# Performance work log

Measured on AMD Instinct MI355X. Metric: run time of the kernel, lower is better.

## Reference

```python
import jax, jax.numpy as jnp
import numpy as np

N_NODES = 100_000
N_EDGES = 3_200_000
IN_DIM, HID_DIM, EMB_DIM = 128, 64, 32


def setup_inputs() -> dict:
    key = jax.random.key(0)
    k0, k1, k2, k3, k4, k5 = jax.random.split(key, 6)
    x = jax.random.normal(k0, (N_NODES, IN_DIM), dtype=jnp.float32)
    edge_index = jax.random.randint(k1, (2, N_EDGES), 0, N_NODES, dtype=jnp.int32)
    # GCNConv parameters (glorot-ish scale)
    W1 = jax.random.normal(k2, (IN_DIM, HID_DIM), dtype=jnp.float32) / np.sqrt(IN_DIM)
    b1 = jnp.zeros((HID_DIM,), dtype=jnp.float32)
    W2 = jax.random.normal(k3, (HID_DIM, EMB_DIM), dtype=jnp.float32) / np.sqrt(HID_DIM)
    b2 = jnp.zeros((EMB_DIM,), dtype=jnp.float32)
    return {"x": x, "W1": W1, "b1": b1, "W2": W2, "b2": b2, "edge_index": edge_index}


def reference(x, W1, b1, W2, b2, edge_index):
    """Two-layer GCN encoder (PyG GCNConv semantics, eval mode so dropout is a no-op).

    Each GCNConv: add self-loops, symmetric deg^-1/2 normalization,
    out = scatter_add(norm_e * (x @ W)[src], dst) + b.
    """
    N = x.shape[0]
    loops = jnp.arange(N, dtype=edge_index.dtype)
    src = jnp.concatenate([edge_index[0], loops])  # [E+N]
    dst = jnp.concatenate([edge_index[1], loops])  # [E+N]

    # degree of destination nodes (self-loops guarantee deg >= 1)
    deg = jax.ops.segment_sum(jnp.ones_like(dst, dtype=jnp.float32), dst,
                              num_segments=N)
    dinv = jax.lax.rsqrt(deg)                      # deg^-1/2, finite since deg>=1
    norm = dinv[src] * dinv[dst]                   # [E+N]

    def gcn_conv(h, W, b):
        h = h @ W                                  # dense transform [N, D_out]
        msg = h[src] * norm[:, None]               # gather + scale [E+N, D_out]
        return jax.ops.segment_sum(msg, dst, num_segments=N) + b

    h = jax.nn.relu(gcn_conv(x, W1, b1))
    # F.dropout with training=False is identity -> omitted
    return gcn_conv(h, W2, b2)
```

## Files before the change

### kernel.cpp

```cpp
#include <hip/hip_runtime.h>

static constexpr int NN = 100000;
static constexpr int NE = 3200000;
static constexpr int DI = 128;
static constexpr int DH = 64;
static constexpr int DO = 32;

static constexpr int NBK  = 391;
static constexpr int BCAP = 9216;
static constexpr int TILE = 8192;
static constexpr int XW1_BASE = 392;
static constexpr int XW1_BLOCKS = (NN + 63) / 64;

typedef short short8 __attribute__((ext_vector_type(8)));
typedef float f32x4  __attribute__((ext_vector_type(4)));

__device__ __forceinline__ unsigned short f2bf(float f) {
    union { float f; unsigned u; } v; v.f = f;
    unsigned r = v.u + 0x7FFFu + ((v.u >> 16) & 1u);
    return (unsigned short)(r >> 16);
}
__device__ __forceinline__ float bflo(unsigned u) {
    union { unsigned u; float f; } v; v.u = u << 16; return v.f;
}
__device__ __forceinline__ float bfhi(unsigned u) {
    union { unsigned u; float f; } v; v.u = u & 0xFFFF0000u; return v.f;
}

__global__ void k_zero(int* __restrict__ p, int n) {
    int i = blockIdx.x * blockDim.x + threadIdx.x;
    if (i < n) p[i] = 0;
}

__global__ __launch_bounds__(256) void k_mega(
        const int* __restrict__ src, const int* __restrict__ dst,
        int* __restrict__ bcur, int* __restrict__ bstore,
        const float* __restrict__ x, const float* __restrict__ W1,
        const float* __restrict__ W2,
        unsigned short* __restrict__ w2bf, unsigned short* __restrict__ h1b) {
    __shared__ int hist[NBK];
    __shared__ int lcur[NBK];
    __shared__ int gpos[NBK];
    __shared__ int stage[TILE];
    __shared__ unsigned short bid[TILE];

    int tid = threadIdx.x;

    if (blockIdx.x < NBK) {
        for (int i = tid; i < NBK; i += 256) hist[i] = 0;
        __syncthreads();

        int base = blockIdx.x * TILE;
        int p[32]; unsigned short bb[32];
#pragma unroll
        for (int k = 0; k < 32; ++k) {
            int e = base + k * 256 + tid;
            if (e < NE) {
                int d = dst[e], s = src[e];
                bb[k] = (unsigned short)(d >> 8);
                p[k]  = ((d & 255) << 24) | s;
                atomicAdd(&hist[bb[k]], 1);
            } else bb[k] = 0xFFFF;
        }
        __syncthreads();

        for (int i = tid; i < NBK; i += 256)
            gpos[i] = atomicAdd(&bcur[i], hist[i]);
        __syncthreads();

        if (tid < 64) {
            int carry = 0;
            for (int c = 0; c < (NBK + 63) / 64; ++c) {
                int idx = c * 64 + tid;
                int v = (idx < NBK) ? hist[idx] : 0;
                int inc = v;
#pragma unroll
                for (int o = 1; o < 64; o <<= 1) {
                    int u = __shfl_up(inc, o, 64);
                    if (tid >= o) inc += u;
                }
                int tot = __shfl(inc, 63, 64);
                if (idx < NBK) { int ex = carry + inc - v; hist[idx] = ex; lcur[idx] = ex; }
                carry += tot;
            }
        }
        __syncthreads();

#pragma unroll
        for (int k = 0; k < 32; ++k) {
            if (bb[k] != 0xFFFF) {
                int lp = atomicAdd(&lcur[bb[k]], 1);
                stage[lp] = p[k];
                bid[lp] = bb[k];
            }
        }
        __syncthreads();

        int tcnt = min(TILE, NE - base);
        for (int i = tid; i < tcnt; i += 256) {
            int b = bid[i];
            int off = gpos[b] + (i - hist[b]);
            if (off < BCAP) bstore[b * BCAP + off] = stage[i];
        }
    } else if (blockIdx.x == NBK) {
        for (int i = tid; i < DH * DO; i += 256) w2bf[i] = f2bf(W2[i]);
    } else {
        int wave = tid >> 6, lane = tid & 63;
        int q = lane >> 4, m = lane & 15, o0 = wave * 16;
        int nb = (blockIdx.x - XW1_BASE) * 64;

        short8 bfr[4];
#pragma unroll
        for (int kb = 0; kb < 4; ++kb)
#pragma unroll
            for (int j = 0; j < 8; ++j)
                bfr[kb][j] = (short)f2bf(W1[(kb * 32 + q * 8 + j) * DH + o0 + m]);

#pragma unroll
        for (int mt = 0; mt < 4; ++mt) {
            int row = min(nb + mt * 16 + m, NN - 1);
            const float* xr = x + (size_t)row * DI;
            f32x4 acc = {0.f, 0.f, 0.f, 0.f};
#pragma unroll
            for (int kb = 0; kb < 4; ++kb) {
                f32x4 u0 = *(const f32x4*)(xr + kb * 32 + q * 8);
                f32x4 u1 = *(const f32x4*)(xr + kb * 32 + q * 8 + 4);
                short8 a;
                a[0] = (short)f2bf(u0.x); a[1] = (short)f2bf(u0.y);
                a[2] = (short)f2bf(u0.z); a[3] = (short)f2bf(u0.w);
                a[4] = (short)f2bf(u1.x); a[5] = (short)f2bf(u1.y);
                a[6] = (short)f2bf(u1.z); a[7] = (short)f2bf(u1.w);
                acc = __builtin_amdgcn_mfma_f32_16x16x32_bf16(a, bfr[kb], acc, 0, 0, 0);
            }
#pragma unroll
            for (int r = 0; r < 4; ++r) {
                int n = nb + mt * 16 + q * 4 + r;
                if (n < NN) h1b[(size_t)n * DH + o0 + m] = f2bf(acc[r]);
            }
        }
    }
}

__global__ __launch_bounds__(512) void k_bsort(
        const int* __restrict__ bcur, int* __restrict__ bstore,
        int* __restrict__ rpb, int* __restrict__ rpe, float* __restrict__ dinv) {
    __shared__ int buf[BCAP];
    __shared__ int sorted[BCAP];
    __shared__ int hist[256], scan[256], cur[256];

    int b = blockIdx.x, tid = threadIdx.x;
    int cnt = min(bcur[b], BCAP);
    int base = b * BCAP;
    for (int i = tid; i < cnt; i += 512) buf[i] = bstore[base + i];
    if (tid < 256) hist[tid] = 0;
    __syncthreads();
    for (int i = tid; i < cnt; i += 512)
        atomicAdd(&hist[((unsigned)buf[i]) >> 24], 1);
    __syncthreads();

    if (tid < 64) {
        int carry = 0;
        for (int c = 0; c < 4; ++c) {
            int idx = c * 64 + tid;
            int v = hist[idx];
            int inc = v;
#pragma unroll
            for (int o = 1; o < 64; o <<= 1) {
                int u = __shfl_up(inc, o, 64);
                if (tid >= o) inc += u;
            }
            int tot = __shfl(inc, 63, 64);
            scan[idx] = carry + inc - v;
            cur[idx]  = carry + inc - v;
            carry += tot;
        }
    }
    __syncthreads();

    if (tid < 256) {
        int n = b * 256 + tid;
        if (n < NN) {
            int beg = base + scan[tid];
            rpb[n] = beg;
            rpe[n] = beg + hist[tid];
            dinv[n] = rsqrtf(1.0f + (float)hist[tid]);
        }
    }

    for (int i = tid; i < cnt; i += 512) {
        unsigned pv = (unsigned)buf[i];
        int pos = atomicAdd(&cur[pv >> 24], 1);
        sorted[pos] = (int)(pv & 0xFFFFFF);
    }
    __syncthreads();
    for (int i = tid; i < cnt; i += 512) bstore[base + i] = sorted[i];
}

__global__ __launch_bounds__(256) void k_gather64(
        const int* __restrict__ rpb, const int* __restrict__ rpe,
        const int* __restrict__ csr, const unsigned* __restrict__ h,
        const float* __restrict__ dinv, const float* __restrict__ b1,
        unsigned* __restrict__ tbf) {
    int wave = threadIdx.x >> 6, lane = threadIdx.x & 63;
    int q = lane >> 4, f4 = lane & 15;
    int n = blockIdx.x * 4 + wave;
    int beg = rpb[n], end = rpe[n];
    float dn = dinv[n];

    float s0 = 0.f, s1 = 0.f, s2 = 0.f, s3 = 0.f;
    if (q == 0) {
        uint2 u = *(const uint2*)(h + (size_t)n * 32 + 2 * f4);
        s0 = bflo(u.x) * dn; s1 = bfhi(u.x) * dn;
        s2 = bflo(u.y) * dn; s3 = bfhi(u.y) * dn;
    }
    for (int c = beg; c < end; c += 64) {
        int cnt = min(64, end - c);
        int sidx = (lane < cnt) ? csr[c + lane] : 0;
        int j = 0;
        for (; j + 8 <= cnt; j += 8) {
            int sa = __shfl(sidx, j + q, 64);
            int sb = __shfl(sidx, j + 4 + q, 64);
            float da = dinv[sa], db = dinv[sb];
            uint2 ua = *(const uint2*)(h + (size_t)sa * 32 + 2 * f4);
            uint2 ub = *(const uint2*)(h + (size_t)sb * 32 + 2 * f4);
            s0 = fmaf(bflo(ua.x), da, s0); s1 = fmaf(bfhi(ua.x), da, s1);
            s2 = fmaf(bflo(ua.y), da, s2); s3 = fmaf(bfhi(ua.y), da, s3);
            s0 = fmaf(bflo(ub.x), db, s0); s1 = fmaf(bfhi(ub.x), db, s1);
            s2 = fmaf(bflo(ub.y), db, s2); s3 = fmaf(bfhi(ub.y), db, s3);
        }
        for (; j < cnt; j += 4) {
            int slot = j + q;
            int s = __shfl(sidx, slot, 64);
            if (slot < cnt) {
                float dv = dinv[s];
                uint2 u = *(const uint2*)(h + (size_t)s * 32 + 2 * f4);
                s0 = fmaf(bflo(u.x), dv, s0); s1 = fmaf(bfhi(u.x), dv, s1);
                s2 = fmaf(bflo(u.y), dv, s2); s3 = fmaf(bfhi(u.y), dv, s3);
            }
        }
    }
    s0 += __shfl_xor(s0, 32, 64); s1 += __shfl_xor(s1, 32, 64);
    s2 += __shfl_xor(s2, 32, 64); s3 += __shfl_xor(s3, 32, 64);
    s0 += __shfl_xor(s0, 16, 64); s1 += __shfl_xor(s1, 16, 64);
    s2 += __shfl_xor(s2, 16, 64); s3 += __shfl_xor(s3, 16, 64);
    if (q == 0) {
        float t0 = fmaxf(fmaf(s0, dn, b1[4 * f4 + 0]), 0.f);
        float t1 = fmaxf(fmaf(s1, dn, b1[4 * f4 + 1]), 0.f);
        float t2 = fmaxf(fmaf(s2, dn, b1[4 * f4 + 2]), 0.f);
        float t3 = fmaxf(fmaf(s3, dn, b1[4 * f4 + 3]), 0.f);
        uint2 o;
        o.x = (unsigned)f2bf(t0) | ((unsigned)f2bf(t1) << 16);
        o.y = (unsigned)f2bf(t2) | ((unsigned)f2bf(t3) << 16);
        *(uint2*)(tbf + (size_t)n * 32 + 2 * f4) = o;
    }
}

__global__ __launch_bounds__(256) void k_l2_mfma(
        const unsigned short* __restrict__ tbf, const unsigned short* __restrict__ w2bf,
        const float* __restrict__ dinv, unsigned short* __restrict__ h2b) {
    int wave = threadIdx.x >> 6, lane = threadIdx.x & 63;
    int q = lane >> 4, m = lane & 15;
    int o0 = (wave & 1) * 16, mt = wave >> 1;
    int nb = blockIdx.x * 32;

    short8 bf[2];
#pragma unroll
    for (int kb = 0; kb < 2; ++kb)
#pragma unroll
        for (int j = 0; j < 8; ++j)
            bf[kb][j] = (short)w2bf[(kb * 32 + q * 8 + j) * DO + o0 + m];

    int row = nb + mt * 16 + m;
    f32x4 acc = {0.f, 0.f, 0.f, 0.f};
#pragma unroll
    for (int kb = 0; kb < 2; ++kb) {
        short8 a = *(const short8*)(tbf + (size_t)row * DH + kb * 32 + q * 8);
        acc = __builtin_amdgcn_mfma_f32_16x16x32_bf16(a, bf[kb], acc, 0, 0, 0);
    }
#pragma unroll
    for (int r = 0; r < 4; ++r) {
        int n = nb + mt * 16 + q * 4 + r;
        if (n < NN) h2b[(size_t)n * DO + o0 + m] = f2bf(acc[r] * dinv[n]);
    }
}

__global__ __launch_bounds__(256) void k_gather32(
        const int* __restrict__ rpb, const int* __restrict__ rpe,
        const int* __restrict__ csr, const unsigned* __restrict__ h,
        const float* __restrict__ dinv, const float* __restrict__ b2,
        float* __restrict__ out) {
    int wave = threadIdx.x >> 6, lane = threadIdx.x & 63;
    int q = lane >> 3, f4 = lane & 7;
    int n = blockIdx.x * 4 + wave;
    int beg = rpb[n], end = rpe[n];

    float s0 = 0.f, s1 = 0.f, s2 = 0.f, s3 = 0.f;
    if (q == 0) {
        uint2 u = *(const uint2*)(h + (size_t)n * 16 + 2 * f4);
        s0 = bflo(u.x); s1 = bfhi(u.x); s2 = bflo(u.y); s3 = bfhi(u.y);
    }
    for (int c = beg; c < end; c += 64) {
        int cnt = min(64, end - c);
        int sidx = (lane < cnt) ? csr[c + lane] : 0;
        int j = 0;
        for (; j + 16 <= cnt; j += 16) {
            int sa = __shfl(sidx, j + q, 64);
            int sb = __shfl(sidx, j + 8 + q, 64);
            uint2 ua = *(const uint2*)(h + (size_t)sa * 16 + 2 * f4);
            uint2 ub = *(const uint2*)(h + (size_t)sb * 16 + 2 * f4);
            s0 += bflo(ua.x); s1 += bfhi(ua.x); s2 += bflo(ua.y); s3 += bfhi(ua.y);
            s0 += bflo(ub.x); s1 += bfhi(ub.x); s2 += bflo(ub.y); s3 += bfhi(ub.y);
        }
        for (; j < cnt; j += 8) {
            int slot = j + q;
            int s = __shfl(sidx, slot, 64);
            if (slot < cnt) {
                uint2 u = *(const uint2*)(h + (size_t)s * 16 + 2 * f4);
                s0 += bflo(u.x); s1 += bfhi(u.x); s2 += bflo(u.y); s3 += bfhi(u.y);
            }
        }
    }
    s0 += __shfl_xor(s0, 32, 64); s1 += __shfl_xor(s1, 32, 64);
    s2 += __shfl_xor(s2, 32, 64); s3 += __shfl_xor(s3, 32, 64);
    s0 += __shfl_xor(s0, 16, 64); s1 += __shfl_xor(s1, 16, 64);
    s2 += __shfl_xor(s2, 16, 64); s3 += __shfl_xor(s3, 16, 64);
    s0 += __shfl_xor(s0, 8, 64);  s1 += __shfl_xor(s1, 8, 64);
    s2 += __shfl_xor(s2, 8, 64);  s3 += __shfl_xor(s3, 8, 64);
    if (q == 0) {
        float dn = dinv[n];
        size_t o = (size_t)n * 32 + 4 * f4;
        out[o + 0] = fmaf(s0, dn, b2[4 * f4 + 0]);
        out[o + 1] = fmaf(s1, dn, b2[4 * f4 + 1]);
        out[o + 2] = fmaf(s2, dn, b2[4 * f4 + 2]);
        out[o + 3] = fmaf(s3, dn, b2[4 * f4 + 3]);
    }
}

extern "C" void kernel_launch(void* const* d_in, const int* in_sizes, int n_in,
                              void* d_out, int out_size, void* d_ws, size_t ws_size,
                              hipStream_t stream) {
    const float* x  = (const float*)d_in[0];
    const float* W1 = (const float*)d_in[1];
    const float* b1 = (const float*)d_in[2];
    const float* W2 = (const float*)d_in[3];
    const float* b2 = (const float*)d_in[4];
    const int* ei  = (const int*)d_in[5];
    const int* src = ei;
    const int* dst = ei + NE;
    float* out = (float*)d_out;

    float* ws    = (float*)d_ws;
    int*   rpb   = (int*)ws;
    int*   rpe   = (int*)(ws + 100352);
    float* dinv  = ws + 200704;
    int*   bcur  = (int*)(ws + 301056);
    int*   bstor = (int*)(ws + 301568);
    unsigned short* w2bf = (unsigned short*)(ws + 3905024);
    unsigned short* tbf  = (unsigned short*)(ws + 3906048);
    unsigned short* h1b  = (unsigned short*)(ws + 7106048);
    unsigned short* h2b  = h1b;

    k_zero     <<<2, 256, 0, stream>>>(bcur, 512);
    k_mega     <<<XW1_BASE + XW1_BLOCKS, 256, 0, stream>>>(
                    src, dst, bcur, bstor, x, W1, W2, w2bf, h1b);
    k_bsort    <<<NBK, 512, 0, stream>>>(bcur, bstor, rpb, rpe, dinv);

    k_gather64 <<<NN / 4, 256, 0, stream>>>(rpb, rpe, bstor, (const unsigned*)h1b,
                                            dinv, b1, (unsigned*)tbf);
    k_l2_mfma  <<<NN / 32, 256, 0, stream>>>(tbf, w2bf, dinv, h2b);
    k_gather32 <<<NN / 4, 256, 0, stream>>>(rpb, rpe, bstor, (const unsigned*)h2b,
                                            dinv, b2, out);
}
```

Measured before the change: 274.7 us.

## Halve bucket tile, scatter sorted CSR directly, widen gather loads to 16 bytes

The edge-bucketing tile drops from 8192 to 4096 edges, which doubles the block count and halves the shared-memory staging. The bucket sort now writes sorted indices straight to a separate CSR buffer instead of going through a second shared array, removing a barrier and cutting LDS use so more blocks fit per CU. Both gather kernels now read 8 bf16 features per lane with uint4 loads, covering more neighbours per wave iteration, and write outputs as vectors. The cost is an extra workspace buffer and more reduction shuffles. Direct global scatter writes are also less coalesced than the old staged copy.

```diff
diff --git a/kernel.cpp b/kernel.cpp
--- a/kernel.cpp
+++ b/kernel.cpp
@@ -8,8 +8,9 @@
 
 static constexpr int NBK  = 391;
 static constexpr int BCAP = 9216;
-static constexpr int TILE = 8192;
-static constexpr int XW1_BASE = 392;
+static constexpr int TILE = 4096;
+static constexpr int NBT  = (NE + TILE - 1) / TILE;
+static constexpr int XW1_BASE = NBT + 1;
 static constexpr int XW1_BLOCKS = (NN + 63) / 64;
 
 typedef short short8 __attribute__((ext_vector_type(8)));
@@ -25,6 +26,13 @@
 }
 __device__ __forceinline__ float bfhi(unsigned u) {
     union { unsigned u; float f; } v; v.u = u & 0xFFFF0000u; return v.f;
+}
+__device__ __forceinline__ void acc_row8(float* s, const unsigned* p, float d) {
+    uint4 u = *(const uint4*)p;
+    s[0] = fmaf(bflo(u.x), d, s[0]); s[1] = fmaf(bfhi(u.x), d, s[1]);
+    s[2] = fmaf(bflo(u.y), d, s[2]); s[3] = fmaf(bfhi(u.y), d, s[3]);
+    s[4] = fmaf(bflo(u.z), d, s[4]); s[5] = fmaf(bfhi(u.z), d, s[5]);
+    s[6] = fmaf(bflo(u.w), d, s[6]); s[7] = fmaf(bfhi(u.w), d, s[7]);
 }
 
 __global__ void k_zero(int* __restrict__ p, int n) {
@@ -46,14 +54,14 @@
 
     int tid = threadIdx.x;
 
-    if (blockIdx.x < NBK) {
+    if (blockIdx.x < NBT) {
         for (int i = tid; i < NBK; i += 256) hist[i] = 0;
         __syncthreads();
 
         int base = blockIdx.x * TILE;
-        int p[32]; unsigned short bb[32];
-#pragma unroll
-        for (int k = 0; k < 32; ++k) {
+        int p[16]; unsigned short bb[16];
+#pragma unroll
+        for (int k = 0; k < 16; ++k) {
             int e = base + k * 256 + tid;
             if (e < NE) {
                 int d = dst[e], s = src[e];
@@ -87,7 +95,7 @@
         __syncthreads();
 
 #pragma unroll
-        for (int k = 0; k < 32; ++k) {
+        for (int k = 0; k < 16; ++k) {
             if (bb[k] != 0xFFFF) {
                 int lp = atomicAdd(&lcur[bb[k]], 1);
                 stage[lp] = p[k];
@@ -102,7 +110,7 @@
             int off = gpos[b] + (i - hist[b]);
             if (off < BCAP) bstore[b * BCAP + off] = stage[i];
         }
-    } else if (blockIdx.x == NBK) {
+    } else if (blockIdx.x == NBT) {
         for (int i = tid; i < DH * DO; i += 256) w2bf[i] = f2bf(W2[i]);
     } else {
         int wave = tid >> 6, lane = tid & 63;
@@ -142,10 +150,10 @@
 }
 
 __global__ __launch_bounds__(512) void k_bsort(
-        const int* __restrict__ bcur, int* __restrict__ bstore,
+        const int* __restrict__ bcur, const int* __restrict__ bstore,
+        int* __restrict__ csr,
         int* __restrict__ rpb, int* __restrict__ rpe, float* __restrict__ dinv) {
     __shared__ int buf[BCAP];
-    __shared__ int sorted[BCAP];
     __shared__ int hist[256], scan[256], cur[256];
 
     int b = blockIdx.x, tid = threadIdx.x;
@@ -190,10 +198,8 @@
     for (int i = tid; i < cnt; i += 512) {
         unsigned pv = (unsigned)buf[i];
         int pos = atomicAdd(&cur[pv >> 24], 1);
-        sorted[pos] = (int)(pv & 0xFFFFFF);
-    }
-    __syncthreads();
-    for (int i = tid; i < cnt; i += 512) bstore[base + i] = sorted[i];
+        csr[base + pos] = (int)(pv & 0xFFFFFF);
+    }
 }
 
 __global__ __launch_bounds__(256) void k_gather64(
@@ -202,56 +208,50 @@
         const float* __restrict__ dinv, const float* __restrict__ b1,
         unsigned* __restrict__ tbf) {
     int wave = threadIdx.x >> 6, lane = threadIdx.x & 63;
-    int q = lane >> 4, f4 = lane & 15;
+    int q = lane >> 3, f8 = lane & 7;
     int n = blockIdx.x * 4 + wave;
     int beg = rpb[n], end = rpe[n];
     float dn = dinv[n];
 
-    float s0 = 0.f, s1 = 0.f, s2 = 0.f, s3 = 0.f;
-    if (q == 0) {
-        uint2 u = *(const uint2*)(h + (size_t)n * 32 + 2 * f4);
-        s0 = bflo(u.x) * dn; s1 = bfhi(u.x) * dn;
-        s2 = bflo(u.y) * dn; s3 = bfhi(u.y) * dn;
-    }
+    float s[8] = {0.f, 0.f, 0.f, 0.f, 0.f, 0.f, 0.f, 0.f};
+    if (q == 0)
+        acc_row8(s, h + (size_t)n * 32 + 4 * f8, dn);
+
     for (int c = beg; c < end; c += 64) {
         int cnt = min(64, end - c);
         int sidx = (lane < cnt) ? csr[c + lane] : 0;
         int j = 0;
-        for (; j + 8 <= cnt; j += 8) {
+        for (; j + 16 <= cnt; j += 16) {
             int sa = __shfl(sidx, j + q, 64);
-            int sb = __shfl(sidx, j + 4 + q, 64);
+            int sb = __shfl(sidx, j + 8 + q, 64);
             float da = dinv[sa], db = dinv[sb];
-            uint2 ua = *(const uint2*)(h + (size_t)sa * 32 + 2 * f4);
-            uint2 ub = *(const uint2*)(h + (size_t)sb * 32 + 2 * f4);
-            s0 = fmaf(bflo(ua.x), da, s0); s1 = fmaf(bfhi(ua.x), da, s1);
-            s2 = fmaf(bflo(ua.y), da, s2); s3 = fmaf(bfhi(ua.y), da, s3);
-            s0 = fmaf(bflo(ub.x), db, s0); s1 = fmaf(bfhi(ub.x), db, s1);
-            s2 = fmaf(bflo(ub.y), db, s2); s3 = fmaf(bfhi(ub.y), db, s3);
-        }
-        for (; j < cnt; j += 4) {
+            acc_row8(s, h + (size_t)sa * 32 + 4 * f8, da);
+            acc_row8(s, h + (size_t)sb * 32 + 4 * f8, db);
+        }
+        for (; j < cnt; j += 8) {
             int slot = j + q;
-            int s = __shfl(sidx, slot, 64);
-            if (slot < cnt) {
-                float dv = dinv[s];
-                uint2 u = *(const uint2*)(h + (size_t)s * 32 + 2 * f4);
-                s0 = fmaf(bflo(u.x), dv, s0); s1 = fmaf(bfhi(u.x), dv, s1);
-                s2 = fmaf(bflo(u.y), dv, s2); s3 = fmaf(bfhi(u.y), dv, s3);
-            }
-        }
-    }
-    s0 += __shfl_xor(s0, 32, 64); s1 += __shfl_xor(s1, 32, 64);
-    s2 += __shfl_xor(s2, 32, 64); s3 += __shfl_xor(s3, 32, 64);
-    s0 += __shfl_xor(s0, 16, 64); s1 += __shfl_xor(s1, 16, 64);
-    s2 += __shfl_xor(s2, 16, 64); s3 += __shfl_xor(s3, 16, 64);
+            int sidx2 = __shfl(sidx, slot, 64);
+            if (slot < cnt)
+                acc_row8(s, h + (size_t)sidx2 * 32 + 4 * f8, dinv[sidx2]);
+        }
+    }
+#pragma unroll
+    for (int r = 0; r < 8; ++r) {
+        s[r] += __shfl_xor(s[r], 8, 64);
+        s[r] += __shfl_xor(s[r], 16, 64);
+        s[r] += __shfl_xor(s[r], 32, 64);
+    }
     if (q == 0) {
-        float t0 = fmaxf(fmaf(s0, dn, b1[4 * f4 + 0]), 0.f);
-        float t1 = fmaxf(fmaf(s1, dn, b1[4 * f4 + 1]), 0.f);
-        float t2 = fmaxf(fmaf(s2, dn, b1[4 * f4 + 2]), 0.f);
-        float t3 = fmaxf(fmaf(s3, dn, b1[4 * f4 + 3]), 0.f);
-        uint2 o;
-        o.x = (unsigned)f2bf(t0) | ((unsigned)f2bf(t1) << 16);
-        o.y = (unsigned)f2bf(t2) | ((unsigned)f2bf(t3) << 16);
-        *(uint2*)(tbf + (size_t)n * 32 + 2 * f4) = o;
+        float t[8];
+#pragma unroll
+        for (int r = 0; r < 8; ++r)
+            t[r] = fmaxf(fmaf(s[r], dn, b1[8 * f8 + r]), 0.f);
+        uint4 o;
+        o.x = (unsigned)f2bf(t[0]) | ((unsigned)f2bf(t[1]) << 16);
+        o.y = (unsigned)f2bf(t[2]) | ((unsigned)f2bf(t[3]) << 16);
+        o.z = (unsigned)f2bf(t[4]) | ((unsigned)f2bf(t[5]) << 16);
+        o.w = (unsigned)f2bf(t[6]) | ((unsigned)f2bf(t[7]) << 16);
+        *(uint4*)(tbf + (size_t)n * 32 + 4 * f8) = o;
     }
 }
 
@@ -290,49 +290,51 @@
         const float* __restrict__ dinv, const float* __restrict__ b2,
         float* __restrict__ out) {
     int wave = threadIdx.x >> 6, lane = threadIdx.x & 63;
-    int q = lane >> 3, f4 = lane & 7;
+    int q = lane >> 2, fi = lane & 3;
     int n = blockIdx.x * 4 + wave;
     int beg = rpb[n], end = rpe[n];
 
-    float s0 = 0.f, s1 = 0.f, s2 = 0.f, s3 = 0.f;
-    if (q == 0) {
-        uint2 u = *(const uint2*)(h + (size_t)n * 16 + 2 * f4);
-        s0 = bflo(u.x); s1 = bfhi(u.x); s2 = bflo(u.y); s3 = bfhi(u.y);
-    }
+    float s[8] = {0.f, 0.f, 0.f, 0.f, 0.f, 0.f, 0.f, 0.f};
+    if (q == 0)
+        acc_row8(s, h + (size_t)n * 16 + 4 * fi, 1.0f);
+
     for (int c = beg; c < end; c += 64) {
         int cnt = min(64, end - c);
         int sidx = (lane < cnt) ? csr[c + lane] : 0;
         int j = 0;
-        for (; j + 16 <= cnt; j += 16) {
+        for (; j + 32 <= cnt; j += 32) {
             int sa = __shfl(sidx, j + q, 64);
-            int sb = __shfl(sidx, j + 8 + q, 64);
-            uint2 ua = *(const uint2*)(h + (size_t)sa * 16 + 2 * f4);
-            uint2 ub = *(const uint2*)(h + (size_t)sb * 16 + 2 * f4);
-            s0 += bflo(ua.x); s1 += bfhi(ua.x); s2 += bflo(ua.y); s3 += bfhi(ua.y);
-            s0 += bflo(ub.x); s1 += bfhi(ub.x); s2 += bflo(ub.y); s3 += bfhi(ub.y);
-        }
-        for (; j < cnt; j += 8) {
+            int sb = __shfl(sidx, j + 16 + q, 64);
+            acc_row8(s, h + (size_t)sa * 16 + 4 * fi, 1.0f);
+            acc_row8(s, h + (size_t)sb * 16 + 4 * fi, 1.0f);
+        }
+        for (; j < cnt; j += 16) {
             int slot = j + q;
-            int s = __shfl(sidx, slot, 64);
-            if (slot < cnt) {
-                uint2 u = *(const uint2*)(h + (size_t)s * 16 + 2 * f4);
-                s0 += bflo(u.x); s1 += bfhi(u.x); s2 += bflo(u.y); s3 += bfhi(u.y);
-            }
-        }
-    }
-    s0 += __shfl_xor(s0, 32, 64); s1 += __shfl_xor(s1, 32, 64);
-    s2 += __shfl_xor(s2, 32, 64); s3 += __shfl_xor(s3, 32, 64);
-    s0 += __shfl_xor(s0, 16, 64); s1 += __shfl_xor(s1, 16, 64);
-    s2 += __shfl_xor(s2, 16, 64); s3 += __shfl_xor(s3, 16, 64);
-    s0 += __shfl_xor(s0, 8, 64);  s1 += __shfl_xor(s1, 8, 64);
-    s2 += __shfl_xor(s2, 8, 64);  s3 += __shfl_xor(s3, 8, 64);
+            int sidx2 = __shfl(sidx, slot, 64);
+            if (slot < cnt)
+                acc_row8(s, h + (size_t)sidx2 * 16 + 4 * fi, 1.0f);
+        }
+    }
+#pragma unroll
+    for (int r = 0; r < 8; ++r) {
+        s[r] += __shfl_xor(s[r], 4, 64);
+        s[r] += __shfl_xor(s[r], 8, 64);
+        s[r] += __shfl_xor(s[r], 16, 64);
+        s[r] += __shfl_xor(s[r], 32, 64);
+    }
     if (q == 0) {
         float dn = dinv[n];
-        size_t o = (size_t)n * 32 + 4 * f4;
-        out[o + 0] = fmaf(s0, dn, b2[4 * f4 + 0]);
-        out[o + 1] = fmaf(s1, dn, b2[4 * f4 + 1]);
-        out[o + 2] = fmaf(s2, dn, b2[4 * f4 + 2]);
-        out[o + 3] = fmaf(s3, dn, b2[4 * f4 + 3]);
+        float4 o0v, o1v;
+        o0v.x = fmaf(s[0], dn, b2[8 * fi + 0]);
+        o0v.y = fmaf(s[1], dn, b2[8 * fi + 1]);
+        o0v.z = fmaf(s[2], dn, b2[8 * fi + 2]);
+        o0v.w = fmaf(s[3], dn, b2[8 * fi + 3]);
+        o1v.x = fmaf(s[4], dn, b2[8 * fi + 4]);
+        o1v.y = fmaf(s[5], dn, b2[8 * fi + 5]);
+        o1v.z = fmaf(s[6], dn, b2[8 * fi + 6]);
+        o1v.w = fmaf(s[7], dn, b2[8 * fi + 7]);
+        *(float4*)(out + (size_t)n * 32 + 8 * fi)     = o0v;
+        *(float4*)(out + (size_t)n * 32 + 8 * fi + 4) = o1v;
     }
 }
 
@@ -355,19 +357,20 @@
     float* dinv  = ws + 200704;
     int*   bcur  = (int*)(ws + 301056);
     int*   bstor = (int*)(ws + 301568);
-    unsigned short* w2bf = (unsigned short*)(ws + 3905024);
-    unsigned short* tbf  = (unsigned short*)(ws + 3906048);
-    unsigned short* h1b  = (unsigned short*)(ws + 7106048);
+    int*   csr   = (int*)(ws + 3905024);
+    unsigned short* w2bf = (unsigned short*)(ws + 7508480);
+    unsigned short* tbf  = (unsigned short*)(ws + 7509504);
+    unsigned short* h1b  = (unsigned short*)(ws + 10709504);
     unsigned short* h2b  = h1b;
 
     k_zero     <<<2, 256, 0, stream>>>(bcur, 512);
     k_mega     <<<XW1_BASE + XW1_BLOCKS, 256, 0, stream>>>(
                     src, dst, bcur, bstor, x, W1, W2, w2bf, h1b);
-    k_bsort    <<<NBK, 512, 0, stream>>>(bcur, bstor, rpb, rpe, dinv);
-
-    k_gather64 <<<NN / 4, 256, 0, stream>>>(rpb, rpe, bstor, (const unsigned*)h1b,
+    k_bsort    <<<NBK, 512, 0, stream>>>(bcur, bstor, csr, rpb, rpe, dinv);
+
+    k_gather64 <<<NN / 4, 256, 0, stream>>>(rpb, rpe, csr, (const unsigned*)h1b,
                                             dinv, b1, (unsigned*)tbf);
     k_l2_mfma  <<<NN / 32, 256, 0, stream>>>(tbf, w2bf, dinv, h2b);
-    k_gather32 <<<NN / 4, 256, 0, stream>>>(rpb, rpe, bstor, (const unsigned*)h2b,
+    k_gather32 <<<NN / 4, 256, 0, stream>>>(rpb, rpe, csr, (const unsigned*)h2b,
                                             dinv, b2, out);
 }
```

After: 278.4 us. No clear change (+1.4%).
